# Optimization experiments

Hardware: AMD Instinct MI355X
Metric: run time of the kernel (lower is better)

The kernel has to match this reference:

```python
import jax, jax.numpy as jnp
import numpy as np
import math

HIDDEN = 768
HEADS = 12
HEAD_DIM = HIDDEN // HEADS  # 64
SEQ = 197
K_RANK = min(128, HEAD_DIM)  # 64
BATCH = 64


def setup_inputs() -> dict:
    key = jax.random.key(0)
    ks = jax.random.split(key, 12)
    init = 0.02
    # Linear weights stored [in, out] (equivalent to torch W.T)
    return {
        "hidden_states": jax.random.normal(ks[0], (BATCH, SEQ, HIDDEN), dtype=jnp.float32),
        "Wq": jax.random.normal(ks[1], (HIDDEN, HIDDEN), dtype=jnp.float32) * init,
        "bq": jnp.zeros((HIDDEN,), dtype=jnp.float32),
        "Wk": jax.random.normal(ks[2], (HIDDEN, HIDDEN), dtype=jnp.float32) * init,
        "bk": jnp.zeros((HIDDEN,), dtype=jnp.float32),
        "Wv": jax.random.normal(ks[3], (HIDDEN, HIDDEN), dtype=jnp.float32) * init,
        "bv": jnp.zeros((HIDDEN,), dtype=jnp.float32),
        "Wo": jax.random.normal(ks[4], (HIDDEN, HIDDEN), dtype=jnp.float32) * init,
        "bo": jnp.zeros((HIDDEN,), dtype=jnp.float32),
        "E_k": jax.random.normal(ks[5], (SEQ, K_RANK), dtype=jnp.float32) * init,
        "E_v": jax.random.normal(ks[6], (SEQ, K_RANK), dtype=jnp.float32) * init,
    }


def reference(hidden_states, Wq, bq, Wk, bk, Wv, bv, Wo, bo, E_k, E_v):
    B, S, D = hidden_states.shape
    H, d = HEADS, HEAD_DIM
    scale = 1.0 / math.sqrt(d)

    def split_heads(x):  # [B,S,D] -> [B,H,S,d]
        return x.reshape(B, S, H, d).transpose(0, 2, 1, 3)

    q = split_heads(hidden_states @ Wq + bq)
    k = split_heads(hidden_states @ Wk + bk)
    v = split_heads(hidden_states @ Wv + bv)

    # low-rank projection of K/V along the sequence axis: [B,H,k,d]
    pk = jnp.einsum('sk,bhsd->bhkd', E_k, k)
    pv = jnp.einsum('sk,bhsd->bhkd', E_v, v)

    # scores over reduced axis: [B,H,S,k]
    scores = jnp.einsum('bhsd,bhkd->bhsk', q, pk) * scale
    probs = jax.nn.softmax(scores, axis=-1)

    ctx = jnp.einsum('bhsk,bhkd->bhsd', probs, pv)
    ctx = ctx.transpose(0, 2, 1, 3).reshape(B, S, D)
    out = ctx @ Wo + bo  # dropout rate 0.0 -> identity
    return out
```

## Files before the change

### kernel.cpp

```cpp
#include <hip/hip_runtime.h>
#include <math.h>

#define B_   64
#define S_   197
#define D_   768
#define H_   12
#define HD_  64
#define M_   (B_ * S_)
#define MPAD 12672
#define KE   224
#define BH_  (B_ * H_)
#define WSZ  ((size_t)D_ * D_)

typedef _Float16 half8_t __attribute__((ext_vector_type(8)));
typedef _Float16 half4_t __attribute__((ext_vector_type(4)));
typedef _Float16 half2_t __attribute__((ext_vector_type(2)));
typedef float floatx4 __attribute__((ext_vector_type(4)));

#define LDS_DMA16(gptr, lptr) \
  __builtin_amdgcn_global_load_lds((const __attribute__((address_space(1))) void*)(gptr), \
                                   (__attribute__((address_space(3))) void*)(lptr), 16, 0, 0)

__global__ __launch_bounds__(256) void prep_y_kernel(
    const float* __restrict__ X,
    const float* __restrict__ Wq, const float* __restrict__ Wk,
    const float* __restrict__ Wv, const float* __restrict__ Wo,
    const float* __restrict__ Ek, const float* __restrict__ Ev,
    _Float16* __restrict__ Xh,
    _Float16* __restrict__ Tcat, _Float16* __restrict__ To,
    float* __restrict__ esumK, float* __restrict__ esumV,
    _Float16* __restrict__ Ybuf)
{
    __shared__ _Float16 smem[KE * 66];
    const int bid = blockIdx.x, tid = threadIdx.x;

    int task, idx;
    if (bid < 9984) {
        const int q = bid / 13, r = bid - q * 13;
        if (r == 0) { task = 0; idx = q; }
        else        { task = 1; idx = 12 * q + r - 1; }
    } else if (bid < 10272) { task = 1; idx = 9216 + (bid - 9984); }
    else if (bid < 12576)   { task = 2; idx = bid - 10272; }
    else                    { task = 3; idx = bid - 12576; }

    if (task == 1) {
        const int i4 = (idx * 256 + tid) * 4;
        float4 v = make_float4(0.f, 0.f, 0.f, 0.f);
        if (i4 < M_ * D_) v = *(const float4*)&X[i4];
        half4_t o = { (_Float16)v.x, (_Float16)v.y, (_Float16)v.z, (_Float16)v.w };
        *(half4_t*)&Xh[i4] = o;
        return;
    }

    if (task == 2) {
        float (*tile)[33] = (float (*)[33])smem;
        const int z = idx / 576, rem = idx % 576;
        const int bx = rem % 24, by = rem / 24;
        const float* W = (z == 0) ? Wk : (z == 1) ? Wv : (z == 2) ? Wq : Wo;
        _Float16* T = (z < 3) ? (Tcat + (size_t)z * WSZ) : To;
        const int n0 = bx * 32, k0 = by * 32;
        const int r = tid >> 3, c4 = (tid & 7) * 4;
        *(float4*)&tile[r][c4] = *(const float4*)&W[(size_t)(k0 + r) * D_ + n0 + c4];
        __syncthreads();
        half4_t o = { (_Float16)tile[c4 + 0][r], (_Float16)tile[c4 + 1][r],
                      (_Float16)tile[c4 + 2][r], (_Float16)tile[c4 + 3][r] };
        *(half4_t*)&T[(size_t)(n0 + r) * D_ + k0 + c4] = o;
        return;
    }

    if (task == 3) {
        const float* E = idx ? Ev : Ek;
        float* es = idx ? esumV : esumK;
        if (tid < 64) {
            float acc = 0.f;
            for (int s = 0; s < S_; ++s) acc += E[s * 64 + tid];
            es[tid] = acc;
        }
        return;
    }

    _Float16* Xs = smem;
    const int b = idx / 12, n0 = (idx % 12) * 64;
    const int w = tid >> 6, lane = tid & 63;
    const int l15 = lane & 15, quad = lane >> 4;

    #pragma unroll
    for (int i = 0; i < 7; ++i) {
        const int s = i * 32 + (tid >> 3);
        const int d0 = (tid & 7) * 8;
        float4 v0 = make_float4(0.f, 0.f, 0.f, 0.f), v1 = v0;
        if (s < S_) {
            const float* src = &X[(size_t)(b * S_ + s) * D_ + n0 + d0];
            v0 = *(const float4*)src;
            v1 = *(const float4*)(src + 4);
        }
        const _Float16 h[8] = { (_Float16)v0.x, (_Float16)v0.y, (_Float16)v0.z,
                                (_Float16)v0.w, (_Float16)v1.x, (_Float16)v1.y,
                                (_Float16)v1.z, (_Float16)v1.w };
        #pragma unroll
        for (int jj = 0; jj < 4; ++jj) {
            half2_t t2 = { h[2 * jj], h[2 * jj + 1] };
            *(half2_t*)&Xs[s * 66 + d0 + 2 * jj] = t2;
        }
    }
    __syncthreads();

    floatx4 acc[2][4] = {};
    #pragma unroll
    for (int k7 = 0; k7 < 7; ++k7) {
        half8_t af[2];
        #pragma unroll
        for (int mi = 0; mi < 2; ++mi) {
            const int row = w * 32 + mi * 16 + l15;
            const float* Esrc = (row < 64) ? Ek : Ev;
            const int er = row & 63;
            #pragma unroll
            for (int jj = 0; jj < 8; ++jj) {
                const int s = k7 * 32 + quad * 8 + jj;
                af[mi][jj] = (_Float16)((s < S_) ? Esrc[s * 64 + er] : 0.f);
            }
        }
        #pragma unroll
        for (int ni = 0; ni < 4; ++ni) {
            const int sb = k7 * 32 + quad * 8;
            half8_t bf;
            #pragma unroll
            for (int jj = 0; jj < 8; ++jj) bf[jj] = Xs[(sb + jj) * 66 + ni * 16 + l15];
            #pragma unroll
            for (int mi = 0; mi < 2; ++mi)
                acc[mi][ni] = __builtin_amdgcn_mfma_f32_16x16x32_f16(
                    af[mi], bf, acc[mi][ni], 0, 0, 0);
        }
    }

    #pragma unroll
    for (int mi = 0; mi < 2; ++mi)
        #pragma unroll
        for (int ni = 0; ni < 4; ++ni)
            #pragma unroll
            for (int i = 0; i < 4; ++i) {
                const int m_local = w * 32 + mi * 16 + quad * 4 + i;
                const int row = (m_local >> 6) * 4096 + b * 64 + (m_local & 63);
                Ybuf[(size_t)row * D_ + n0 + ni * 16 + l15] = (_Float16)acc[mi][ni][i];
            }
}

__global__ __launch_bounds__(256) void gemm_qpkv(
    const _Float16* __restrict__ Xh, const _Float16* __restrict__ Ybuf,
    const _Float16* __restrict__ Tcat,
    const float* __restrict__ bq, const float* __restrict__ bk,
    const float* __restrict__ bv,
    const float* __restrict__ esumK, const float* __restrict__ esumV,
    _Float16* __restrict__ Qh, _Float16* __restrict__ pk16,
    _Float16* __restrict__ pv16)
{
    __shared__ _Float16 sm[16384];
    const int bid = blockIdx.x;
    const _Float16 *A, *W;
    const float *bias, *esum;
    _Float16* O16;
    int m0, n0, rowb;
    if (bid < 624) {
        const int xcd = bid & 7, t = bid >> 3;
        const int slot = t / 6, j = t - slot * 6;
        const int m_blk = slot * 8 + xcd;
        if (m_blk >= MPAD / 128) return;
        m0 = m_blk * 128; n0 = j * 128; rowb = m0;
        A = Xh; W = Tcat + 2 * WSZ + (size_t)n0 * D_;
        bias = bq; esum = nullptr; O16 = Qh;
    } else {
        const int b2 = bid - 624;
        const int xcd = b2 & 7, t = b2 >> 3;
        const int slot = t / 6, j = t - slot * 6;
        const int m_blk = slot * 8 + xcd;
        m0 = m_blk * 128; n0 = j * 128;
        const bool pv = (m_blk >= 32);
        rowb = pv ? m0 - 4096 : m0;
        A = Ybuf; W = Tcat + (pv ? WSZ : 0) + (size_t)n0 * D_;
        bias = pv ? bv : bk; esum = pv ? esumV : esumK;
        O16 = pv ? pv16 : pk16;
    }

    const int tid = threadIdx.x;
    const int w = tid >> 6, lane = tid & 63;
    const int fr = lane & 15, quad = lane >> 4, f7 = lane & 7;
    const int l3 = lane >> 3;
    const int csrc = ((lane & 7) ^ l3) * 8;
    const int wm = (w >> 1) * 64, wn = (w & 1) * 64;

    const _Float16* Abase = A + (size_t)(m0 + w * 32 + l3) * D_ + csrc;
    const _Float16* Wbase = W + (size_t)(w * 32 + l3) * D_ + csrc;

    floatx4 acc[4][4] = {};

    for (int k0 = 0; k0 < D_; k0 += 64) {
        #pragma unroll
        for (int j = 0; j < 4; ++j) {
            LDS_DMA16(Abase + (size_t)(j * 8) * D_ + k0, &sm[w * 2048 + j * 512]);
            LDS_DMA16(Wbase + (size_t)(j * 8) * D_ + k0, &sm[8192 + w * 2048 + j * 512]);
        }
        __syncthreads();
        #pragma unroll
        for (int ksub = 0; ksub < 2; ++ksub) {
            const int sa = ((ksub * 4 + quad) ^ f7) * 8;
            half8_t af[4], bf[4];
            #pragma unroll
            for (int i = 0; i < 4; ++i) {
                af[i] = *(const half8_t*)&sm[(wm + i * 16 + fr) * 64 + sa];
                bf[i] = *(const half8_t*)&sm[8192 + (wn + i * 16 + fr) * 64 + sa];
            }
            #pragma unroll
            for (int mi = 0; mi < 4; ++mi)
                #pragma unroll
                for (int ni = 0; ni < 4; ++ni)
                    acc[mi][ni] = __builtin_amdgcn_mfma_f32_16x16x32_f16(
                        af[mi], bf[ni], acc[mi][ni], 0, 0, 0);
        }
        __syncthreads();
    }

    float bval[4];
    #pragma unroll
    for (int ni = 0; ni < 4; ++ni)
        bval[ni] = bias[n0 + wn + ni * 16 + fr];

    _Float16* ct = &sm[w * 2176];
    #pragma unroll
    for (int half = 0; half < 2; ++half) {
        #pragma unroll
        for (int mi2 = 0; mi2 < 2; ++mi2) {
            const int mi = half * 2 + mi2;
            float esv[4] = {1.f, 1.f, 1.f, 1.f};
            if (esum) {
                const float4 es4 = *(const float4*)&esum[mi * 16 + quad * 4];
                esv[0] = es4.x; esv[1] = es4.y; esv[2] = es4.z; esv[3] = es4.w;
            }
            #pragma unroll
            for (int ni = 0; ni < 4; ++ni)
                #pragma unroll
                for (int i = 0; i < 4; ++i)
                    ct[(mi2 * 16 + quad * 4 + i) * 68 + ni * 16 + fr] =
                        (_Float16)(acc[mi][ni][i] + esv[i] * bval[ni]);
        }
        #pragma unroll
        for (int pass = 0; pass < 4; ++pass) {
            const int rr = pass * 8 + (lane >> 3);
            const int cc = (lane & 7) * 8;
            const half8_t v = *(const half8_t*)&ct[rr * 68 + cc];
            *(half8_t*)&O16[(size_t)(rowb + wm + half * 32 + rr) * D_ + n0 + wn + cc] = v;
        }
    }
}

__global__ __launch_bounds__(256) void gemm_o(
    const _Float16* __restrict__ CTX, const _Float16* __restrict__ To,
    const float* __restrict__ bo, float* __restrict__ O32)
{
    __shared__ _Float16 sm[16384];
    const int xcd = blockIdx.x & 7, t = blockIdx.x >> 3;
    const int slot = t / 6, j = t - slot * 6;
    const int m_blk = slot * 8 + xcd;
    if (m_blk >= MPAD / 128) return;
    const int m0 = m_blk * 128, n0 = j * 128;

    const int tid = threadIdx.x;
    const int w = tid >> 6, lane = tid & 63;
    const int fr = lane & 15, quad = lane >> 4, f7 = lane & 7;
    const int l3 = lane >> 3;
    const int csrc = ((lane & 7) ^ l3) * 8;
    const int wm = (w >> 1) * 64, wn = (w & 1) * 64;

    const _Float16* Abase = CTX + (size_t)(m0 + w * 32 + l3) * D_ + csrc;
    const _Float16* Wbase = To + (size_t)(n0 + w * 32 + l3) * D_ + csrc;

    floatx4 acc[4][4] = {};

    for (int k0 = 0; k0 < D_; k0 += 64) {
        #pragma unroll
        for (int j2 = 0; j2 < 4; ++j2) {
            LDS_DMA16(Abase + (size_t)(j2 * 8) * D_ + k0, &sm[w * 2048 + j2 * 512]);
            LDS_DMA16(Wbase + (size_t)(j2 * 8) * D_ + k0, &sm[8192 + w * 2048 + j2 * 512]);
        }
        __syncthreads();
        #pragma unroll
        for (int ksub = 0; ksub < 2; ++ksub) {
            const int sa = ((ksub * 4 + quad) ^ f7) * 8;
            half8_t af[4], bf[4];
            #pragma unroll
            for (int i = 0; i < 4; ++i) {
                af[i] = *(const half8_t*)&sm[(wm + i * 16 + fr) * 64 + sa];
                bf[i] = *(const half8_t*)&sm[8192 + (wn + i * 16 + fr) * 64 + sa];
            }
            #pragma unroll
            for (int mi = 0; mi < 4; ++mi)
                #pragma unroll
                for (int ni = 0; ni < 4; ++ni)
                    acc[mi][ni] = __builtin_amdgcn_mfma_f32_16x16x32_f16(
                        af[mi], bf[ni], acc[mi][ni], 0, 0, 0);
        }
        __syncthreads();
    }

    float bval[4];
    #pragma unroll
    for (int ni = 0; ni < 4; ++ni)
        bval[ni] = bo[n0 + wn + ni * 16 + fr];

    const bool full = (m0 + 128 <= M_);
    #pragma unroll
    for (int ni = 0; ni < 4; ++ni) {
        const int n = n0 + wn + ni * 16 + fr;
        #pragma unroll
        for (int mi = 0; mi < 4; ++mi)
            #pragma unroll
            for (int i = 0; i < 4; ++i) {
                const int m = m0 + wm + mi * 16 + quad * 4 + i;
                if (full || m < M_)
                    O32[(size_t)m * D_ + n] = acc[mi][ni][i] + bval[ni];
            }
    }
}

__global__ __launch_bounds__(256) void attn_kernel(
    const _Float16* __restrict__ Qh, const _Float16* __restrict__ pk16,
    const _Float16* __restrict__ pv16, _Float16* __restrict__ CTXh)
{
    __shared__ _Float16 P[64 * 80];
    const int bh = blockIdx.x, b = bh / H_, h = bh % H_;
    const int tid = threadIdx.x, w = tid >> 6, lane = tid & 63;
    const int l15 = lane & 15, quad = lane >> 4;
    const _Float16* pkB = pk16 + (size_t)(b * 64) * D_ + h * 64;
    const _Float16* pvB = pv16 + (size_t)(b * 64) * D_ + h * 64;
    const size_t qbase = (size_t)(b * S_) * D_ + h * HD_;

    half8_t bkf[4][2], bvf[4][2];
    #pragma unroll
    for (int ni = 0; ni < 4; ++ni)
        #pragma unroll
        for (int kk = 0; kk < 2; ++kk) {
            bkf[ni][kk] = *(const half8_t*)&pkB[(size_t)(ni * 16 + l15) * D_ + kk * 32 + quad * 8];
            #pragma unroll
            for (int jj = 0; jj < 8; ++jj)
                bvf[ni][kk][jj] = pvB[(size_t)(kk * 32 + quad * 8 + jj) * D_ + ni * 16 + l15];
        }

    for (int t = w; t < 13; t += 4) {
        const int srow = t * 16;
        floatx4 acc[4] = {};
        #pragma unroll
        for (int kk = 0; kk < 2; ++kk) {
            const half8_t aq = *(const half8_t*)
                &Qh[qbase + (size_t)(srow + l15) * D_ + kk * 32 + quad * 8];
            #pragma unroll
            for (int ni = 0; ni < 4; ++ni)
                acc[ni] = __builtin_amdgcn_mfma_f32_16x16x32_f16(
                    aq, bkf[ni][kk], acc[ni], 0, 0, 0);
        }
        float p[4][4];
        #pragma unroll
        for (int i = 0; i < 4; ++i) {
            const float s0 = acc[0][i] * 0.125f, s1 = acc[1][i] * 0.125f;
            const float s2 = acc[2][i] * 0.125f, s3 = acc[3][i] * 0.125f;
            float mx = fmaxf(fmaxf(s0, s1), fmaxf(s2, s3));
            #pragma unroll
            for (int off = 1; off < 16; off <<= 1)
                mx = fmaxf(mx, __shfl_xor(mx, off, 64));
            const float e0 = __expf(s0 - mx), e1 = __expf(s1 - mx);
            const float e2 = __expf(s2 - mx), e3 = __expf(s3 - mx);
            float sme = e0 + e1 + e2 + e3;
            #pragma unroll
            for (int off = 1; off < 16; off <<= 1)
                sme += __shfl_xor(sme, off, 64);
            const float inv = 1.f / sme;
            p[0][i] = e0 * inv; p[1][i] = e1 * inv;
            p[2][i] = e2 * inv; p[3][i] = e3 * inv;
        }
        #pragma unroll
        for (int ni = 0; ni < 4; ++ni)
            #pragma unroll
            for (int i = 0; i < 4; ++i)
                P[(w * 16 + quad * 4 + i) * 80 + ni * 16 + l15] = (_Float16)p[ni][i];

        floatx4 accv[4] = {};
        #pragma unroll
        for (int kk = 0; kk < 2; ++kk) {
            const half8_t ap = *(const half8_t*)&P[(w * 16 + l15) * 80 + kk * 32 + quad * 8];
            #pragma unroll
            for (int ni = 0; ni < 4; ++ni)
                accv[ni] = __builtin_amdgcn_mfma_f32_16x16x32_f16(
                    ap, bvf[ni][kk], accv[ni], 0, 0, 0);
        }
        #pragma unroll
        for (int ni = 0; ni < 4; ++ni)
            #pragma unroll
            for (int i = 0; i < 4; ++i) {
                const int s = srow + quad * 4 + i;
                if (s < S_)
                    CTXh[qbase + (size_t)s * D_ + ni * 16 + l15] = (_Float16)accv[ni][i];
            }
    }
}

extern "C" void kernel_launch(void* const* d_in, const int* in_sizes, int n_in,
                              void* d_out, int out_size, void* d_ws, size_t ws_size,
                              hipStream_t stream) {
    const float* X   = (const float*)d_in[0];
    const float* Wq  = (const float*)d_in[1];
    const float* bq  = (const float*)d_in[2];
    const float* Wk  = (const float*)d_in[3];
    const float* bk  = (const float*)d_in[4];
    const float* Wv  = (const float*)d_in[5];
    const float* bv  = (const float*)d_in[6];
    const float* Wo  = (const float*)d_in[7];
    const float* bo  = (const float*)d_in[8];
    const float* E_k = (const float*)d_in[9];
    const float* E_v = (const float*)d_in[10];
    float* out = (float*)d_out;

    char* p = (char*)d_ws;
    _Float16* Xh   = (_Float16*)p; p += (size_t)MPAD * D_ * 2;
    _Float16* Tcat = (_Float16*)p; p += (size_t)3 * WSZ * 2;
    _Float16* To   = (_Float16*)p; p += (size_t)WSZ * 2;
    _Float16* Qh   = (_Float16*)p; p += (size_t)MPAD * D_ * 2;
    float* esumK   = (float*)p;    p += 64 * sizeof(float);
    float* esumV   = (float*)p;    p += 64 * sizeof(float);
    _Float16* Ybuf = (_Float16*)p; p += (size_t)8192 * D_ * 2;
    _Float16* pk16 = (_Float16*)p; p += (size_t)4096 * D_ * 2;
    _Float16* pv16 = (_Float16*)p;

    prep_y_kernel<<<12578, 256, 0, stream>>>(X, Wq, Wk, Wv, Wo, E_k, E_v,
                                             Xh, Tcat, To, esumK, esumV, Ybuf);
    gemm_qpkv<<<1008, 256, 0, stream>>>(Xh, Ybuf, Tcat,
                                        bq, bk, bv, esumK, esumV,
                                        Qh, pk16, pv16);
    attn_kernel<<<BH_, 256, 0, stream>>>(Qh, pk16, pv16, Xh);
    gemm_o<<<624, 256, 0, stream>>>(Xh, To, bo, out);
}
```

Measured before the change: 209.4 us.

## Double-buffer LDS tiles in QPKV and output GEMMs to overlap loads with MFMA

Both GEMM kernels now use two LDS buffers. The DMA for the next k-tile is issued before the MFMA compute on the current tile, and the k loop is fully unrolled with a prologue and epilogue. This is meant to hide global-to-LDS load latency behind matrix math and drop one barrier per step. In exchange, LDS use per block doubles to 64KB, which may cut occupancy on the CU.

Measured after the change: 202.0 us. 3.5% less time.

```diff
diff --git a/kernel.cpp b/kernel.cpp
--- a/kernel.cpp
+++ b/kernel.cpp
@@ -154,7 +154,7 @@
     _Float16* __restrict__ Qh, _Float16* __restrict__ pk16,
     _Float16* __restrict__ pv16)
 {
-    __shared__ _Float16 sm[16384];
+    __shared__ _Float16 sm[32768];
     const int bid = blockIdx.x;
     const _Float16 *A, *W;
     const float *bias, *esum;
@@ -193,31 +193,46 @@
 
     floatx4 acc[4][4] = {};
 
-    for (int k0 = 0; k0 < D_; k0 += 64) {
-        #pragma unroll
-        for (int j = 0; j < 4; ++j) {
-            LDS_DMA16(Abase + (size_t)(j * 8) * D_ + k0, &sm[w * 2048 + j * 512]);
-            LDS_DMA16(Wbase + (size_t)(j * 8) * D_ + k0, &sm[8192 + w * 2048 + j * 512]);
-        }
+#define QPKV_STAGE(BUF, K0) \
+    { _Pragma("unroll") \
+      for (int j = 0; j < 4; ++j) { \
+          LDS_DMA16(Abase + (size_t)(j * 8) * D_ + (K0), &sm[(BUF) * 16384 + w * 2048 + j * 512]); \
+          LDS_DMA16(Wbase + (size_t)(j * 8) * D_ + (K0), &sm[(BUF) * 16384 + 8192 + w * 2048 + j * 512]); \
+      } }
+
+#define QPKV_COMPUTE(BUF) \
+    { _Pragma("unroll") \
+      for (int ksub = 0; ksub < 2; ++ksub) { \
+          const int sa = ((ksub * 4 + quad) ^ f7) * 8; \
+          half8_t af[4], bf[4]; \
+          _Pragma("unroll") \
+          for (int i = 0; i < 4; ++i) { \
+              af[i] = *(const half8_t*)&sm[(BUF) * 16384 + (wm + i * 16 + fr) * 64 + sa]; \
+              bf[i] = *(const half8_t*)&sm[(BUF) * 16384 + 8192 + (wn + i * 16 + fr) * 64 + sa]; \
+          } \
+          _Pragma("unroll") \
+          for (int mi = 0; mi < 4; ++mi) \
+              _Pragma("unroll") \
+              for (int ni = 0; ni < 4; ++ni) \
+                  acc[mi][ni] = __builtin_amdgcn_mfma_f32_16x16x32_f16( \
+                      af[mi], bf[ni], acc[mi][ni], 0, 0, 0); \
+      } }
+
+    QPKV_STAGE(0, 0);
+    __syncthreads();
+    #pragma unroll
+    for (int t = 0; t < 10; t += 2) {
+        QPKV_STAGE(1, (t + 1) * 64);
+        QPKV_COMPUTE(0);
         __syncthreads();
-        #pragma unroll
-        for (int ksub = 0; ksub < 2; ++ksub) {
-            const int sa = ((ksub * 4 + quad) ^ f7) * 8;
-            half8_t af[4], bf[4];
-            #pragma unroll
-            for (int i = 0; i < 4; ++i) {
-                af[i] = *(const half8_t*)&sm[(wm + i * 16 + fr) * 64 + sa];
-                bf[i] = *(const half8_t*)&sm[8192 + (wn + i * 16 + fr) * 64 + sa];
-            }
-            #pragma unroll
-            for (int mi = 0; mi < 4; ++mi)
-                #pragma unroll
-                for (int ni = 0; ni < 4; ++ni)
-                    acc[mi][ni] = __builtin_amdgcn_mfma_f32_16x16x32_f16(
-                        af[mi], bf[ni], acc[mi][ni], 0, 0, 0);
-        }
+        QPKV_STAGE(0, (t + 2) * 64);
+        QPKV_COMPUTE(1);
         __syncthreads();
     }
+    QPKV_STAGE(1, 11 * 64);
+    QPKV_COMPUTE(0);
+    __syncthreads();
+    QPKV_COMPUTE(1);
 
     float bval[4];
     #pragma unroll
@@ -256,7 +271,7 @@
     const _Float16* __restrict__ CTX, const _Float16* __restrict__ To,
     const float* __restrict__ bo, float* __restrict__ O32)
 {
-    __shared__ _Float16 sm[16384];
+    __shared__ _Float16 sm[32768];
     const int xcd = blockIdx.x & 7, t = blockIdx.x >> 3;
     const int slot = t / 6, j = t - slot * 6;
     const int m_blk = slot * 8 + xcd;
@@ -275,31 +290,21 @@
 
     floatx4 acc[4][4] = {};
 
-    for (int k0 = 0; k0 < D_; k0 += 64) {
-        #pragma unroll
-        for (int j2 = 0; j2 < 4; ++j2) {
-            LDS_DMA16(Abase + (size_t)(j2 * 8) * D_ + k0, &sm[w * 2048 + j2 * 512]);
-            LDS_DMA16(Wbase + (size_t)(j2 * 8) * D_ + k0, &sm[8192 + w * 2048 + j2 * 512]);
-        }
+    QPKV_STAGE(0, 0);
+    __syncthreads();
+    #pragma unroll
+    for (int t2 = 0; t2 < 10; t2 += 2) {
+        QPKV_STAGE(1, (t2 + 1) * 64);
+        QPKV_COMPUTE(0);
         __syncthreads();
-        #pragma unroll
-        for (int ksub = 0; ksub < 2; ++ksub) {
-            const int sa = ((ksub * 4 + quad) ^ f7) * 8;
-            half8_t af[4], bf[4];
-            #pragma unroll
-            for (int i = 0; i < 4; ++i) {
-                af[i] = *(const half8_t*)&sm[(wm + i * 16 + fr) * 64 + sa];
-                bf[i] = *(const half8_t*)&sm[8192 + (wn + i * 16 + fr) * 64 + sa];
-            }
-            #pragma unroll
-            for (int mi = 0; mi < 4; ++mi)
-                #pragma unroll
-                for (int ni = 0; ni < 4; ++ni)
-                    acc[mi][ni] = __builtin_amdgcn_mfma_f32_16x16x32_f16(
-                        af[mi], bf[ni], acc[mi][ni], 0, 0, 0);
-        }
+        QPKV_STAGE(0, (t2 + 2) * 64);
+        QPKV_COMPUTE(1);
         __syncthreads();
     }
+    QPKV_STAGE(1, 11 * 64);
+    QPKV_COMPUTE(0);
+    __syncthreads();
+    QPKV_COMPUTE(1);
 
     float bval[4];
     #pragma unroll
```
